# Performance work log

Measured on AMD Instinct MI355X. Metric: run time of the kernel, lower is better.

The kernel has to match this reference:

```python
import jax, jax.numpy as jnp
import numpy as np

NEG_SLOPE = 0.01  # F.leaky_relu default


def grid_sample_bilinear(im, pts):
    """torch.nn.functional.grid_sample equivalent, mode='bilinear',
    align_corners=True, padding_mode='zeros'.
    im: [B, C, H, W], pts: [B, N, 2] in [-1, 1] (x, y order). Returns [B, C, N].
    """
    B, C, H, W = im.shape
    x = (pts[..., 0] + 1.0) * 0.5 * (W - 1)  # [B, N]
    y = (pts[..., 1] + 1.0) * 0.5 * (H - 1)
    x0 = jnp.floor(x)
    y0 = jnp.floor(y)
    wx1 = x - x0
    wy1 = y - y0
    wx0 = 1.0 - wx1
    wy0 = 1.0 - wy1
    x0i = x0.astype(jnp.int32)
    y0i = y0.astype(jnp.int32)
    x1i = x0i + 1
    y1i = y0i + 1

    def corner(yi, xi, w):
        valid = (xi >= 0) & (xi < W) & (yi >= 0) & (yi < H)
        yc = jnp.clip(yi, 0, H - 1)
        xc = jnp.clip(xi, 0, W - 1)
        # gather per-batch: [B, C, N]
        g = jax.vmap(lambda f, yy, xx: f[:, yy, xx])(im, yc, xc)
        return g * (w * valid.astype(im.dtype))[:, None, :]

    return (corner(y0i, x0i, wy0 * wx0) + corner(y0i, x1i, wy0 * wx1)
            + corner(y1i, x0i, wy1 * wx0) + corner(y1i, x1i, wy1 * wx1))


def conv1x1(x, w, b):
    # x: [B, Cin, N], w: [Cout, Cin], b: [Cout] -> [B, Cout, N]
    return jnp.einsum('oi,bin->bon', w, x) + b[None, :, None]


def setup_inputs() -> dict:
    key = jax.random.key(0)
    ks = jax.random.split(key, 9)
    B, N, C, H, W = 64, 6890, 256, 56, 56
    filter_channels = [256, 128, 64, 5]
    points = jax.random.uniform(ks[0], (B, N, 2), jnp.float32, -1.0, 1.0)
    im_feat = jax.random.normal(ks[1], (B, C, H, W), jnp.float32)

    def mk_conv(k, cin, cout):
        k1, k2 = jax.random.split(k)
        bound = 1.0 / np.sqrt(cin)
        w = jax.random.uniform(k1, (cout, cin), jnp.float32, -bound, bound)
        b = jax.random.uniform(k2, (cout,), jnp.float32, -bound, bound)
        return w, b

    w0, b0 = mk_conv(ks[2], filter_channels[0], filter_channels[1])
    w1, b1 = mk_conv(ks[3], filter_channels[1] + filter_channels[0], filter_channels[2])
    w2, b2 = mk_conv(ks[4], filter_channels[2] + filter_channels[0], filter_channels[3])
    return {"points": points, "im_feat": im_feat,
            "w0": w0, "b0": b0, "w1": w1, "b1": b1, "w2": w2, "b2": b2}


def reference(points, im_feat, w0, b0, w1, b1, w2, b2):
    # sampling: bilinear gather of point-wise features, [B, C_s, N]
    point_feat = grid_sample_bilinear(im_feat, points)
    # reduce_dim: 1x1 conv MLP with skip-concat of the input features
    y = jax.nn.leaky_relu(conv1x1(point_feat, w0, b0), NEG_SLOPE)
    y = jax.nn.leaky_relu(conv1x1(jnp.concatenate([y, point_feat], axis=1), w1, b1), NEG_SLOPE)
    y = conv1x1(jnp.concatenate([y, point_feat], axis=1), w2, b2)  # last layer: no leaky_relu
    y = jax.nn.relu(y)  # self.last_op
    mesh_align_feat = y.reshape(y.shape[0], -1)  # [B, C_p * N]
    return (mesh_align_feat, point_feat)
```

## Files before the change

kernel.cpp:

```cpp
#include <hip/hip_runtime.h>

#define B_    64
#define C_    256
#define H_    56
#define W_    56
#define N_    6890
#define HW_   3136
#define NTILE 108
#define GPTS  1723
#define PPT   7

#define WB1_OFF (128*256)
#define WB2_OFF (128*256 + 64*384)
#define WTOT    (128*256 + 64*384 + 5*320)

typedef __attribute__((ext_vector_type(8))) __bf16 bf16x8;
typedef __attribute__((ext_vector_type(8))) unsigned short ushort8;
typedef __attribute__((ext_vector_type(4))) float f32x4;
typedef __attribute__((ext_vector_type(2))) float f32x2;
typedef __attribute__((ext_vector_type(4))) unsigned int uint4v;
typedef __attribute__((ext_vector_type(2))) unsigned int uint2v;

__device__ __forceinline__ unsigned short f2bf(float f) {
    unsigned int u = __builtin_bit_cast(unsigned int, f);
    u += 0x7FFFu + ((u >> 16) & 1u);
    return (unsigned short)(u >> 16);
}
__device__ __forceinline__ unsigned int pack2(float lo, float hi) {
    return (unsigned int)f2bf(lo) | ((unsigned int)f2bf(hi) << 16);
}
__device__ __forceinline__ float leaky(float v) { return v > 0.f ? v : 0.01f * v; }

__global__ void wconv_kernel(const float* __restrict__ w0, const float* __restrict__ w1,
                             const float* __restrict__ w2, unsigned short* __restrict__ wb) {
    int i = blockIdx.x * 256 + threadIdx.x;
    if (i >= WTOT) return;
    float v = (i < WB1_OFF) ? w0[i] : (i < WB2_OFF) ? w1[i - WB1_OFF] : w2[i - WB2_OFF];
    wb[i] = f2bf(v);
}

__device__ __forceinline__ void stage_load(f32x4* rs, const float* src, int t) {
#pragma unroll
    for (int k = 0; k < 13; k++) {
        int idx = t + (k << 8);
        f32x4 z = {0.f, 0.f, 0.f, 0.f};
        rs[k] = (idx < 3136) ? ((const f32x4*)src)[idx] : z;
    }
}
__device__ __forceinline__ void stage_write(float* dst, const f32x4* rs, int t) {
#pragma unroll
    for (int k = 0; k < 13; k++) {
        int idx = t + (k << 8);
        if (idx < 3136) ((f32x4*)dst)[idx] = rs[k];
    }
}

__global__ __launch_bounds__(256) void gather_kernel(
    const float* __restrict__ points, const float* __restrict__ im,
    float* __restrict__ out1) {
    __shared__ float Ls[2][4 * HW_];

    const int t   = threadIdx.x;
    const int bid = blockIdx.x;
    const int xcd  = bid & 7;
    const int slot = bid >> 3;
    const int b    = (slot >> 2) * 8 + xcd;
    const int grp  = slot & 3;
    const int nbase = grp * GPTS;

    int   ia0[PPT], ia1[PPT];
    float wl0[PPT], wr0[PPT], wl1[PPT], wr1[PPT];
#pragma unroll
    for (int p = 0; p < PPT; p++) {
        int ln = t + (p << 8);
        int n  = nbase + ln;
        bool ok = (ln < GPTS) && (n < N_);
        int nl = ok ? n : 0;
        f32x2 pt = *(const f32x2*)(points + ((size_t)b * N_ + nl) * 2);
        float fx = fminf(fmaxf((pt.x + 1.f) * 27.5f, 0.f), 55.f);
        float fy = fminf(fmaxf((pt.y + 1.f) * 27.5f, 0.f), 55.f);
        float x0f = floorf(fx), y0f = floorf(fy);
        int x0 = (int)x0f, y0 = (int)y0f;
        float wx1 = fx - x0f, wy1 = fy - y0f;
        float wx0 = 1.f - wx1, wy0 = 1.f - wy1;
        bool hix = x0 >= W_ - 1;
        int   xb  = hix ? W_ - 2 : x0;
        float wxl = hix ? 0.f : wx0;
        float wxr = hix ? wx0 : wx1;
        int y0c = min(y0, H_ - 1);
        int y1c = min(y0 + 1, H_ - 1);
        float g = ok ? 1.f : 0.f;
        wl0[p] = wy0 * wxl * g; wr0[p] = wy0 * wxr * g;
        wl1[p] = wy1 * wxl * g; wr1[p] = wy1 * wxr * g;
        ia0[p] = y0c * W_ + xb; ia1[p] = y1c * W_ + xb;
    }

    const float* imb = im + (size_t)b * C_ * HW_;
    f32x4 rs[13];

    stage_load(rs, imb, t);
    stage_write(Ls[0], rs, t);
    __syncthreads();

    for (int ch = 0; ch < 64; ch++) {
        const int buf = ch & 1;
        if (ch < 63) stage_load(rs, imb + (size_t)(ch + 1) * 4 * HW_, t);

        const int c0 = ch * 4;
        const float* plane = Ls[buf];
#pragma unroll
        for (int p = 0; p < PPT; p++) {
            int ln = t + (p << 8);
            int n  = nbase + ln;
            bool ok = (ln < GPTS) && (n < N_);
            size_t obase = ((size_t)b * C_ + c0) * N_ + n;
#pragma unroll
            for (int j = 0; j < 4; j++) {
                const float* q = plane + j * HW_;
                float v = wl0[p] * q[ia0[p]] + wr0[p] * q[ia0[p] + 1]
                        + wl1[p] * q[ia1[p]] + wr1[p] * q[ia1[p] + 1];
                if (ok) out1[obase + (size_t)j * N_] = v;
            }
        }
        if (ch < 63) stage_write(Ls[buf ^ 1], rs, t);
        __syncthreads();
    }
}

__device__ __forceinline__ bf16x8 afrag_f32(const float* __restrict__ wp, int ldk,
                                            int rowbase, int k0, int lane, int nrows) {
    int i = rowbase + (lane & 15);
    int k = k0 + ((lane >> 4) << 3);
    ushort8 u;
    if (i < nrows) {
        const float* s = wp + (size_t)i * ldk + k;
#pragma unroll
        for (int j = 0; j < 8; j++) u[j] = f2bf(s[j]);
    } else {
#pragma unroll
        for (int j = 0; j < 8; j++) u[j] = 0;
    }
    return __builtin_bit_cast(bf16x8, u);
}
__device__ __forceinline__ bf16x8 afrag_bf(const unsigned short* __restrict__ wb, int ldk,
                                           int rowbase, int k0, int lane, int nrows) {
    int i = rowbase + (lane & 15);
    int k = k0 + ((lane >> 4) << 3);
    if (i < nrows) return __builtin_bit_cast(bf16x8, *(const ushort8*)(wb + (size_t)i * ldk + k));
    ushort8 z = {0, 0, 0, 0, 0, 0, 0, 0};
    return __builtin_bit_cast(bf16x8, z);
}

__device__ __forceinline__ bf16x8 bfrag(const unsigned int* buf, int rowstride_dw,
                                        int n, int k0) {
    int cd = (k0 >> 1) ^ ((n & 7) << 2);
    uint4v v = *(const uint4v*)(buf + n * rowstride_dw + cd);
    return __builtin_bit_cast(bf16x8, v);
}

template <bool BF16W>
__global__ __launch_bounds__(256) void mlp_kernel(
    const float* __restrict__ pf,
    const float* __restrict__ w0, const float* __restrict__ b0,
    const float* __restrict__ w1, const float* __restrict__ b1,
    const float* __restrict__ w2, const float* __restrict__ b2,
    const unsigned short* __restrict__ wb,
    float* __restrict__ out0) {
    __shared__ unsigned int Xs[64 * 128];
    __shared__ unsigned int Y0s[64 * 64];

    const int t    = threadIdx.x;
    const int lane = t & 63;
    const int wave = t >> 6;
    const int bid  = blockIdx.x;
    const int b    = bid / NTILE;
    const int tile = bid - b * NTILE;
    const int n0   = tile * 64;

    const float* pfb = pf + (size_t)b * C_ * N_;
    const int nn_g = min(n0 + lane, N_ - 1);
    const int swz  = (lane & 7) << 2;
#pragma unroll
    for (int g8 = 0; g8 < 8; g8++) {
        int c0 = wave * 64 + g8 * 8;
        float v[8];
#pragma unroll
        for (int j = 0; j < 8; j++) v[j] = pfb[(size_t)(c0 + j) * N_ + nn_g];
        uint4v pk;
        pk[0] = pack2(v[0], v[1]); pk[1] = pack2(v[2], v[3]);
        pk[2] = pack2(v[4], v[5]); pk[3] = pack2(v[6], v[7]);
        *(uint4v*)(Xs + lane * 128 + ((c0 >> 1) ^ swz)) = pk;
    }

    bf16x8 a1[2][8];
#pragma unroll
    for (int mt = 0; mt < 2; mt++)
#pragma unroll
        for (int ks = 0; ks < 8; ks++)
            a1[mt][ks] = BF16W ? afrag_bf(wb, 256, (wave * 2 + mt) * 16, ks * 32, lane, 1 << 30)
                               : afrag_f32(w0, 256, (wave * 2 + mt) * 16, ks * 32, lane, 1 << 30);

    __syncthreads();

    const int cl = lane & 15;
    const int rh = lane >> 4;
    const int kq = rh << 3;

    f32x4 acc1[2][4] = {};
#pragma unroll
    for (int ks = 0; ks < 8; ks++) {
        bf16x8 bx[4];
#pragma unroll
        for (int nt = 0; nt < 4; nt++)
            bx[nt] = bfrag(Xs, 128, nt * 16 + cl, ks * 32 + kq);
#pragma unroll
        for (int mt = 0; mt < 2; mt++)
#pragma unroll
            for (int nt = 0; nt < 4; nt++)
                acc1[mt][nt] = __builtin_amdgcn_mfma_f32_16x16x32_bf16(
                    a1[mt][ks], bx[nt], acc1[mt][nt], 0, 0, 0);
    }

#pragma unroll
    for (int mt = 0; mt < 2; mt++) {
        int m0 = (wave * 2 + mt) * 16 + (rh << 2);
        f32x4 bias = *(const f32x4*)(b0 + m0);
#pragma unroll
        for (int nt = 0; nt < 4; nt++) {
            int nn = nt * 16 + cl;
            float v0 = leaky(acc1[mt][nt][0] + bias[0]);
            float v1 = leaky(acc1[mt][nt][1] + bias[1]);
            float v2 = leaky(acc1[mt][nt][2] + bias[2]);
            float v3 = leaky(acc1[mt][nt][3] + bias[3]);
            int md = (m0 >> 1) ^ ((nn & 7) << 2);
            uint2v pk; pk[0] = pack2(v0, v1); pk[1] = pack2(v2, v3);
            *(uint2v*)(Y0s + nn * 64 + md) = pk;
        }
    }

    bf16x8 a2[12];
#pragma unroll
    for (int ks = 0; ks < 12; ks++)
        a2[ks] = BF16W ? afrag_bf(wb + WB1_OFF, 384, wave * 16, ks * 32, lane, 1 << 30)
                       : afrag_f32(w1, 384, wave * 16, ks * 32, lane, 1 << 30);

    __syncthreads();

    f32x4 acc2[4] = {};
#pragma unroll
    for (int ks = 0; ks < 12; ks++) {
#pragma unroll
        for (int nt = 0; nt < 4; nt++) {
            bf16x8 bx = (ks < 4) ? bfrag(Y0s, 64, nt * 16 + cl, ks * 32 + kq)
                                 : bfrag(Xs, 128, nt * 16 + cl, (ks - 4) * 32 + kq);
            acc2[nt] = __builtin_amdgcn_mfma_f32_16x16x32_bf16(a2[ks], bx, acc2[nt], 0, 0, 0);
        }
    }

    bf16x8 a3[10];
#pragma unroll
    for (int ks = 0; ks < 10; ks++)
        a3[ks] = BF16W ? afrag_bf(wb + WB2_OFF, 320, 0, ks * 32, lane, 5)
                       : afrag_f32(w2, 320, 0, ks * 32, lane, 5);

    __syncthreads();

    {
        int m0 = wave * 16 + (rh << 2);
        f32x4 bias = *(const f32x4*)(b1 + m0);
#pragma unroll
        for (int nt = 0; nt < 4; nt++) {
            int nn = nt * 16 + cl;
            float v0 = leaky(acc2[nt][0] + bias[0]);
            float v1 = leaky(acc2[nt][1] + bias[1]);
            float v2 = leaky(acc2[nt][2] + bias[2]);
            float v3 = leaky(acc2[nt][3] + bias[3]);
            int md = (m0 >> 1) ^ ((nn & 7) << 2);
            uint2v pk; pk[0] = pack2(v0, v1); pk[1] = pack2(v2, v3);
            *(uint2v*)(Y0s + nn * 32 + md) = pk;
        }
    }

    __syncthreads();

    {
        int nn = wave * 16 + cl;
        f32x4 acc3 = {};
#pragma unroll
        for (int ks = 0; ks < 10; ks++) {
            bf16x8 bx = (ks < 2) ? bfrag(Y0s, 32, nn, ks * 32 + kq)
                                 : bfrag(Xs, 128, nn, (ks - 2) * 32 + kq);
            acc3 = __builtin_amdgcn_mfma_f32_16x16x32_bf16(a3[ks], bx, acc3, 0, 0, 0);
        }
        int gn2 = n0 + nn;
        if (gn2 < N_) {
#pragma unroll
            for (int r = 0; r < 4; r++) {
                int m = (rh << 2) + r;
                if (m < 5) {
                    float v = acc3[r] + b2[m];
                    v = v > 0.f ? v : 0.f;
                    out0[((size_t)b * 5 + m) * N_ + gn2] = v;
                }
            }
        }
    }
}

extern "C" void kernel_launch(void* const* d_in, const int* in_sizes, int n_in,
                              void* d_out, int out_size, void* d_ws, size_t ws_size,
                              hipStream_t stream) {
    const float* points = (const float*)d_in[0];
    const float* im     = (const float*)d_in[1];
    const float* w0     = (const float*)d_in[2];
    const float* b0     = (const float*)d_in[3];
    const float* w1     = (const float*)d_in[4];
    const float* b1     = (const float*)d_in[5];
    const float* w2     = (const float*)d_in[6];
    const float* b2     = (const float*)d_in[7];
    float* out0 = (float*)d_out;
    float* out1 = out0 + (size_t)B_ * 5 * N_;

    const bool use_bf16w = (ws_size >= (size_t)WTOT * 2) && (d_ws != nullptr);
    unsigned short* wb = (unsigned short*)d_ws;

    if (use_bf16w) {
        hipLaunchKernelGGL(wconv_kernel, dim3((WTOT + 255) / 256), dim3(256), 0, stream,
                           w0, w1, w2, wb);
    }
    hipLaunchKernelGGL(gather_kernel, dim3(256), dim3(256), 0, stream,
                       points, im, out1);
    if (use_bf16w) {
        hipLaunchKernelGGL(mlp_kernel<true>, dim3(B_ * NTILE), dim3(256), 0, stream,
                           out1, w0, b0, w1, b1, w2, b2, wb, out0);
    } else {
        hipLaunchKernelGGL(mlp_kernel<false>, dim3(B_ * NTILE), dim3(256), 0, stream,
                           out1, w0, b0, w1, b1, w2, b2, (const unsigned short*)nullptr, out0);
    }
}
```

Measured before the change: 375.8 us.

## Interleave channels in swizzled LDS gather and emit bf16 point features for MLP

New measurement: 482.5 us. 28.4% more time.

```diff
diff --git a/kernel.cpp b/kernel.cpp
--- a/kernel.cpp
+++ b/kernel.cpp
@@ -7,8 +7,9 @@
 #define N_    6890
 #define HW_   3136
 #define NTILE 108
-#define GPTS  1723
-#define PPT   7
+#define GRP_  8
+#define GPTS2 862
+#define PPT2  4
 
 #define WB1_OFF (128*256)
 #define WB2_OFF (128*256 + 64*384)
@@ -30,6 +31,7 @@
     return (unsigned int)f2bf(lo) | ((unsigned int)f2bf(hi) << 16);
 }
 __device__ __forceinline__ float leaky(float v) { return v > 0.f ? v : 0.01f * v; }
+__device__ __forceinline__ int pswz(int p) { return p ^ ((p >> 3) & 7); }
 
 __global__ void wconv_kernel(const float* __restrict__ w0, const float* __restrict__ w1,
                              const float* __restrict__ w2, unsigned short* __restrict__ wb) {
@@ -39,42 +41,27 @@
     wb[i] = f2bf(v);
 }
 
-__device__ __forceinline__ void stage_load(f32x4* rs, const float* src, int t) {
-#pragma unroll
-    for (int k = 0; k < 13; k++) {
-        int idx = t + (k << 8);
-        f32x4 z = {0.f, 0.f, 0.f, 0.f};
-        rs[k] = (idx < 3136) ? ((const f32x4*)src)[idx] : z;
-    }
-}
-__device__ __forceinline__ void stage_write(float* dst, const f32x4* rs, int t) {
-#pragma unroll
-    for (int k = 0; k < 13; k++) {
-        int idx = t + (k << 8);
-        if (idx < 3136) ((f32x4*)dst)[idx] = rs[k];
-    }
-}
-
-__global__ __launch_bounds__(256) void gather_kernel(
+template <bool XP>
+__global__ __launch_bounds__(256, 2) void gather_kernel(
     const float* __restrict__ points, const float* __restrict__ im,
-    float* __restrict__ out1) {
-    __shared__ float Ls[2][4 * HW_];
+    float* __restrict__ out1, unsigned int* __restrict__ x2) {
+    __shared__ float Ls[HW_ * 4];
 
     const int t   = threadIdx.x;
     const int bid = blockIdx.x;
-    const int xcd  = bid & 7;
-    const int slot = bid >> 3;
-    const int b    = (slot >> 2) * 8 + xcd;
-    const int grp  = slot & 3;
-    const int nbase = grp * GPTS;
-
-    int   ia0[PPT], ia1[PPT];
-    float wl0[PPT], wr0[PPT], wl1[PPT], wr1[PPT];
-#pragma unroll
-    for (int p = 0; p < PPT; p++) {
+    const int xcd = bid & 7;
+    const int idx = bid >> 3;
+    const int b   = ((idx & 7) << 3) + xcd;
+    const int grp = idx >> 3;
+    const int nbase = grp * GPTS2;
+
+    int   p00[PPT2], p01[PPT2], p10[PPT2], p11[PPT2];
+    float w00[PPT2], w01[PPT2], w10[PPT2], w11[PPT2];
+#pragma unroll
+    for (int p = 0; p < PPT2; p++) {
         int ln = t + (p << 8);
         int n  = nbase + ln;
-        bool ok = (ln < GPTS) && (n < N_);
+        bool ok = (ln < GPTS2) && (n < N_);
         int nl = ok ? n : 0;
         f32x2 pt = *(const f32x2*)(points + ((size_t)b * N_ + nl) * 2);
         float fx = fminf(fmaxf((pt.x + 1.f) * 27.5f, 0.f), 55.f);
@@ -89,42 +76,75 @@
         float wxr = hix ? wx0 : wx1;
         int y0c = min(y0, H_ - 1);
         int y1c = min(y0 + 1, H_ - 1);
-        float g = ok ? 1.f : 0.f;
-        wl0[p] = wy0 * wxl * g; wr0[p] = wy0 * wxr * g;
-        wl1[p] = wy1 * wxl * g; wr1[p] = wy1 * wxr * g;
-        ia0[p] = y0c * W_ + xb; ia1[p] = y1c * W_ + xb;
-    }
-
-    const float* imb = im + (size_t)b * C_ * HW_;
-    f32x4 rs[13];
-
-    stage_load(rs, imb, t);
-    stage_write(Ls[0], rs, t);
-    __syncthreads();
+        w00[p] = wy0 * wxl; w01[p] = wy0 * wxr;
+        w10[p] = wy1 * wxl; w11[p] = wy1 * wxr;
+        int ia0 = y0c * W_ + xb, ia1 = y1c * W_ + xb;
+        p00[p] = pswz(ia0); p01[p] = pswz(ia0 + 1);
+        p10[p] = pswz(ia1); p11[p] = pswz(ia1 + 1);
+    }
+
+    const f32x4* imb4 = (const f32x4*)(im + (size_t)b * C_ * HW_);
+    f32x4 rs[4][4];
+
+#define GLOAD(CH) {                                                         \
+    _Pragma("unroll")                                                       \
+    for (int k = 0; k < 4; k++) {                                           \
+        int g = t + (k << 8);                                               \
+        if (g < 784) {                                                      \
+            _Pragma("unroll")                                               \
+            for (int j = 0; j < 4; j++)                                     \
+                rs[k][j] = imb4[(size_t)((CH) * 4 + j) * 784 + g];          \
+        }                                                                   \
+    } }
+
+    GLOAD(0);
 
     for (int ch = 0; ch < 64; ch++) {
-        const int buf = ch & 1;
-        if (ch < 63) stage_load(rs, imb + (size_t)(ch + 1) * 4 * HW_, t);
+        __syncthreads();
+#pragma unroll
+        for (int k = 0; k < 4; k++) {
+            int g = t + (k << 8);
+            if (g < 784) {
+#pragma unroll
+                for (int i = 0; i < 4; i++) {
+                    int pi = (g << 2) + i;
+                    f32x4 v = {rs[0][0][0], 0.f, 0.f, 0.f};
+                    v[0] = rs[k][0][i]; v[1] = rs[k][1][i];
+                    v[2] = rs[k][2][i]; v[3] = rs[k][3][i];
+                    *(f32x4*)(Ls + (pswz(pi) << 2)) = v;
+                }
+            }
+        }
+        __syncthreads();
+        if (ch < 63) GLOAD(ch + 1);
 
         const int c0 = ch * 4;
-        const float* plane = Ls[buf];
-#pragma unroll
-        for (int p = 0; p < PPT; p++) {
+#pragma unroll
+        for (int p = 0; p < PPT2; p++) {
+            f32x4 q00 = *(const f32x4*)(Ls + (p00[p] << 2));
+            f32x4 q01 = *(const f32x4*)(Ls + (p01[p] << 2));
+            f32x4 q10 = *(const f32x4*)(Ls + (p10[p] << 2));
+            f32x4 q11 = *(const f32x4*)(Ls + (p11[p] << 2));
+            float v0 = w00[p]*q00[0] + w01[p]*q01[0] + w10[p]*q10[0] + w11[p]*q11[0];
+            float v1 = w00[p]*q00[1] + w01[p]*q01[1] + w10[p]*q10[1] + w11[p]*q11[1];
+            float v2 = w00[p]*q00[2] + w01[p]*q01[2] + w10[p]*q10[2] + w11[p]*q11[2];
+            float v3 = w00[p]*q00[3] + w01[p]*q01[3] + w10[p]*q10[3] + w11[p]*q11[3];
             int ln = t + (p << 8);
             int n  = nbase + ln;
-            bool ok = (ln < GPTS) && (n < N_);
-            size_t obase = ((size_t)b * C_ + c0) * N_ + n;
-#pragma unroll
-            for (int j = 0; j < 4; j++) {
-                const float* q = plane + j * HW_;
-                float v = wl0[p] * q[ia0[p]] + wr0[p] * q[ia0[p] + 1]
-                        + wl1[p] * q[ia1[p]] + wr1[p] * q[ia1[p] + 1];
-                if (ok) out1[obase + (size_t)j * N_] = v;
+            if ((ln < GPTS2) && (n < N_)) {
+                size_t ob = ((size_t)b * C_ + c0) * N_ + n;
+                out1[ob]             = v0;
+                out1[ob + N_]        = v1;
+                out1[ob + 2 * N_]    = v2;
+                out1[ob + 3 * N_]    = v3;
+                if (XP) {
+                    uint2v pk; pk[0] = pack2(v0, v1); pk[1] = pack2(v2, v3);
+                    *(uint2v*)(x2 + ((size_t)((b << 6) + ch) * N_ + n) * 2) = pk;
+                }
             }
         }
-        if (ch < 63) stage_write(Ls[buf ^ 1], rs, t);
-        __syncthreads();
-    }
+    }
+#undef GLOAD
 }
 
 __device__ __forceinline__ bf16x8 afrag_f32(const float* __restrict__ wp, int ldk,
@@ -158,9 +178,9 @@
     return __builtin_bit_cast(bf16x8, v);
 }
 
-template <bool BF16W>
+template <bool XP, bool BF16W>
 __global__ __launch_bounds__(256) void mlp_kernel(
-    const float* __restrict__ pf,
+    const float* __restrict__ pf, const unsigned int* __restrict__ x2,
     const float* __restrict__ w0, const float* __restrict__ b0,
     const float* __restrict__ w1, const float* __restrict__ b1,
     const float* __restrict__ w2, const float* __restrict__ b2,
@@ -177,19 +197,32 @@
     const int tile = bid - b * NTILE;
     const int n0   = tile * 64;
 
-    const float* pfb = pf + (size_t)b * C_ * N_;
     const int nn_g = min(n0 + lane, N_ - 1);
     const int swz  = (lane & 7) << 2;
-#pragma unroll
-    for (int g8 = 0; g8 < 8; g8++) {
-        int c0 = wave * 64 + g8 * 8;
-        float v[8];
-#pragma unroll
-        for (int j = 0; j < 8; j++) v[j] = pfb[(size_t)(c0 + j) * N_ + nn_g];
-        uint4v pk;
-        pk[0] = pack2(v[0], v[1]); pk[1] = pack2(v[2], v[3]);
-        pk[2] = pack2(v[4], v[5]); pk[3] = pack2(v[6], v[7]);
-        *(uint4v*)(Xs + lane * 128 + ((c0 >> 1) ^ swz)) = pk;
+
+    if (XP) {
+#pragma unroll
+        for (int j = 0; j < 8; j++) {
+            int d2a = wave * 16 + 2 * j;
+            const unsigned int* src = x2 + ((size_t)((b << 6) + d2a) * N_ + nn_g) * 2;
+            uint2v q0 = *(const uint2v*)src;
+            uint2v q1 = *(const uint2v*)(src + 2 * (size_t)N_);
+            uint4v pk; pk[0] = q0[0]; pk[1] = q0[1]; pk[2] = q1[0]; pk[3] = q1[1];
+            *(uint4v*)(Xs + lane * 128 + ((wave * 32 + 4 * j) ^ swz)) = pk;
+        }
+    } else {
+        const float* pfb = pf + (size_t)b * C_ * N_;
+#pragma unroll
+        for (int g8 = 0; g8 < 8; g8++) {
+            int c0 = wave * 64 + g8 * 8;
+            float v[8];
+#pragma unroll
+            for (int j = 0; j < 8; j++) v[j] = pfb[(size_t)(c0 + j) * N_ + nn_g];
+            uint4v pk;
+            pk[0] = pack2(v[0], v[1]); pk[1] = pack2(v[2], v[3]);
+            pk[2] = pack2(v[4], v[5]); pk[3] = pack2(v[6], v[7]);
+            *(uint4v*)(Xs + lane * 128 + ((c0 >> 1) ^ swz)) = pk;
+        }
     }
 
     bf16x8 a1[2][8];
@@ -321,20 +354,33 @@
     float* out0 = (float*)d_out;
     float* out1 = out0 + (size_t)B_ * 5 * N_;
 
-    const bool use_bf16w = (ws_size >= (size_t)WTOT * 2) && (d_ws != nullptr);
-    unsigned short* wb = (unsigned short*)d_ws;
-
-    if (use_bf16w) {
+    const size_t XBYTES = (size_t)B_ * 64 * N_ * 2 * 4;
+    const size_t WBYTES = (size_t)WTOT * 2;
+    const bool xok = (d_ws != nullptr) && (ws_size >= XBYTES + WBYTES);
+    const bool wok = xok || ((d_ws != nullptr) && (ws_size >= WBYTES));
+    unsigned int*   x2 = (unsigned int*)d_ws;
+    unsigned short* wb = xok ? (unsigned short*)((char*)d_ws + XBYTES)
+                             : (unsigned short*)d_ws;
+
+    if (wok) {
         hipLaunchKernelGGL(wconv_kernel, dim3((WTOT + 255) / 256), dim3(256), 0, stream,
                            w0, w1, w2, wb);
     }
-    hipLaunchKernelGGL(gather_kernel, dim3(256), dim3(256), 0, stream,
-                       points, im, out1);
-    if (use_bf16w) {
-        hipLaunchKernelGGL(mlp_kernel<true>, dim3(B_ * NTILE), dim3(256), 0, stream,
-                           out1, w0, b0, w1, b1, w2, b2, wb, out0);
+    if (xok) {
+        hipLaunchKernelGGL(gather_kernel<true>, dim3(B_ * GRP_), dim3(256), 0, stream,
+                           points, im, out1, x2);
+        hipLaunchKernelGGL((mlp_kernel<true, true>), dim3(B_ * NTILE), dim3(256), 0, stream,
+                           out1, x2, w0, b0, w1, b1, w2, b2, wb, out0);
     } else {
-        hipLaunchKernelGGL(mlp_kernel<false>, dim3(B_ * NTILE), dim3(256), 0, stream,
-                           out1, w0, b0, w1, b1, w2, b2, (const unsigned short*)nullptr, out0);
-    }
-}
+        hipLaunchKernelGGL(gather_kernel<false>, dim3(B_ * GRP_), dim3(256), 0, stream,
+                           points, im, out1, (unsigned int*)nullptr);
+        if (wok) {
+            hipLaunchKernelGGL((mlp_kernel<false, true>), dim3(B_ * NTILE), dim3(256), 0, stream,
+                               out1, (const unsigned int*)nullptr, w0, b0, w1, b1, w2, b2, wb, out0);
+        } else {
+            hipLaunchKernelGGL((mlp_kernel<false, false>), dim3(B_ * NTILE), dim3(256), 0, stream,
+                               out1, (const unsigned int*)nullptr, w0, b0, w1, b1, w2, b2,
+                               (const unsigned short*)nullptr, out0);
+        }
+    }
+}
```

## Split gather by batch and channel group with interleaved swizzled LDS layout

Applied to the files above, without the earlier changes.

Result: faster. 318.2 us (-15.3%).

```diff
diff --git a/kernel.cpp b/kernel.cpp
--- a/kernel.cpp
+++ b/kernel.cpp
@@ -7,8 +7,6 @@
 #define N_    6890
 #define HW_   3136
 #define NTILE 108
-#define GPTS  1723
-#define PPT   7
 
 #define WB1_OFF (128*256)
 #define WB2_OFF (128*256 + 64*384)
@@ -30,6 +28,7 @@
     return (unsigned int)f2bf(lo) | ((unsigned int)f2bf(hi) << 16);
 }
 __device__ __forceinline__ float leaky(float v) { return v > 0.f ? v : 0.01f * v; }
+__device__ __forceinline__ int pswz(int p) { return p ^ ((p >> 3) & 7); }
 
 __global__ void wconv_kernel(const float* __restrict__ w0, const float* __restrict__ w1,
                              const float* __restrict__ w2, unsigned short* __restrict__ wb) {
@@ -39,91 +38,70 @@
     wb[i] = f2bf(v);
 }
 
-__device__ __forceinline__ void stage_load(f32x4* rs, const float* src, int t) {
-#pragma unroll
-    for (int k = 0; k < 13; k++) {
-        int idx = t + (k << 8);
-        f32x4 z = {0.f, 0.f, 0.f, 0.f};
-        rs[k] = (idx < 3136) ? ((const f32x4*)src)[idx] : z;
-    }
-}
-__device__ __forceinline__ void stage_write(float* dst, const f32x4* rs, int t) {
-#pragma unroll
-    for (int k = 0; k < 13; k++) {
-        int idx = t + (k << 8);
-        if (idx < 3136) ((f32x4*)dst)[idx] = rs[k];
-    }
-}
-
-__global__ __launch_bounds__(256) void gather_kernel(
+__global__ __launch_bounds__(512, 6) void gather_kernel(
     const float* __restrict__ points, const float* __restrict__ im,
     float* __restrict__ out1) {
-    __shared__ float Ls[2][4 * HW_];
+    __shared__ float Ls[HW_ * 4];
 
     const int t   = threadIdx.x;
     const int bid = blockIdx.x;
-    const int xcd  = bid & 7;
-    const int slot = bid >> 3;
-    const int b    = (slot >> 2) * 8 + xcd;
-    const int grp  = slot & 3;
-    const int nbase = grp * GPTS;
-
-    int   ia0[PPT], ia1[PPT];
-    float wl0[PPT], wr0[PPT], wl1[PPT], wr1[PPT];
-#pragma unroll
-    for (int p = 0; p < PPT; p++) {
-        int ln = t + (p << 8);
-        int n  = nbase + ln;
-        bool ok = (ln < GPTS) && (n < N_);
-        int nl = ok ? n : 0;
-        f32x2 pt = *(const f32x2*)(points + ((size_t)b * N_ + nl) * 2);
-        float fx = fminf(fmaxf((pt.x + 1.f) * 27.5f, 0.f), 55.f);
-        float fy = fminf(fmaxf((pt.y + 1.f) * 27.5f, 0.f), 55.f);
-        float x0f = floorf(fx), y0f = floorf(fy);
-        int x0 = (int)x0f, y0 = (int)y0f;
-        float wx1 = fx - x0f, wy1 = fy - y0f;
-        float wx0 = 1.f - wx1, wy0 = 1.f - wy1;
-        bool hix = x0 >= W_ - 1;
-        int   xb  = hix ? W_ - 2 : x0;
-        float wxl = hix ? 0.f : wx0;
-        float wxr = hix ? wx0 : wx1;
-        int y0c = min(y0, H_ - 1);
-        int y1c = min(y0 + 1, H_ - 1);
-        float g = ok ? 1.f : 0.f;
-        wl0[p] = wy0 * wxl * g; wr0[p] = wy0 * wxr * g;
-        wl1[p] = wy1 * wxl * g; wr1[p] = wy1 * wxr * g;
-        ia0[p] = y0c * W_ + xb; ia1[p] = y1c * W_ + xb;
-    }
-
-    const float* imb = im + (size_t)b * C_ * HW_;
-    f32x4 rs[13];
-
-    stage_load(rs, imb, t);
-    stage_write(Ls[0], rs, t);
-    __syncthreads();
-
-    for (int ch = 0; ch < 64; ch++) {
-        const int buf = ch & 1;
-        if (ch < 63) stage_load(rs, imb + (size_t)(ch + 1) * 4 * HW_, t);
-
-        const int c0 = ch * 4;
-        const float* plane = Ls[buf];
-#pragma unroll
-        for (int p = 0; p < PPT; p++) {
-            int ln = t + (p << 8);
-            int n  = nbase + ln;
-            bool ok = (ln < GPTS) && (n < N_);
-            size_t obase = ((size_t)b * C_ + c0) * N_ + n;
-#pragma unroll
-            for (int j = 0; j < 4; j++) {
-                const float* q = plane + j * HW_;
-                float v = wl0[p] * q[ia0[p]] + wr0[p] * q[ia0[p] + 1]
-                        + wl1[p] * q[ia1[p]] + wr1[p] * q[ia1[p] + 1];
-                if (ok) out1[obase + (size_t)j * N_] = v;
+    const int b  = ((bid & 7) << 3) | ((bid >> 3) & 7);
+    const int ch = bid >> 6;
+
+    const f32x4* im4 = (const f32x4*)(im + ((size_t)b * C_ + ch * 4) * HW_);
+#pragma unroll
+    for (int g0 = 0; g0 < 2; g0++) {
+        int g = t + (g0 << 9);
+        if (g < 784) {
+            f32x4 r0 = im4[g];
+            f32x4 r1 = im4[784 + g];
+            f32x4 r2 = im4[1568 + g];
+            f32x4 r3 = im4[2352 + g];
+#pragma unroll
+            for (int i = 0; i < 4; i++) {
+                f32x4 v; v[0] = r0[i]; v[1] = r1[i]; v[2] = r2[i]; v[3] = r3[i];
+                *(f32x4*)(Ls + (pswz((g << 2) + i) << 2)) = v;
             }
         }
-        if (ch < 63) stage_write(Ls[buf ^ 1], rs, t);
-        __syncthreads();
+    }
+    __syncthreads();
+
+    const float* ptb = points + (size_t)b * N_ * 2;
+    const size_t ob0 = ((size_t)b * C_ + ch * 4) * N_;
+#pragma unroll 2
+    for (int p = 0; p < 14; p++) {
+        int n = t + (p << 9);
+        if (n < N_) {
+            f32x2 pt = *(const f32x2*)(ptb + 2 * n);
+            float fx = fminf(fmaxf((pt.x + 1.f) * 27.5f, 0.f), 55.f);
+            float fy = fminf(fmaxf((pt.y + 1.f) * 27.5f, 0.f), 55.f);
+            float x0f = floorf(fx), y0f = floorf(fy);
+            int x0 = (int)x0f, y0 = (int)y0f;
+            float wx1 = fx - x0f, wy1 = fy - y0f;
+            float wx0 = 1.f - wx1, wy0 = 1.f - wy1;
+            bool hix = x0 >= W_ - 1;
+            int   xb  = hix ? W_ - 2 : x0;
+            float wxl = hix ? 0.f : wx0;
+            float wxr = hix ? wx0 : wx1;
+            int y0c = min(y0, H_ - 1);
+            int y1c = min(y0 + 1, H_ - 1);
+            float w00 = wy0 * wxl, w01 = wy0 * wxr;
+            float w10 = wy1 * wxl, w11 = wy1 * wxr;
+            int ia0 = y0c * W_ + xb, ia1 = y1c * W_ + xb;
+
+            f32x4 q00 = *(const f32x4*)(Ls + (pswz(ia0)     << 2));
+            f32x4 q01 = *(const f32x4*)(Ls + (pswz(ia0 + 1) << 2));
+            f32x4 q10 = *(const f32x4*)(Ls + (pswz(ia1)     << 2));
+            f32x4 q11 = *(const f32x4*)(Ls + (pswz(ia1 + 1) << 2));
+            float v0 = w00*q00[0] + w01*q01[0] + w10*q10[0] + w11*q11[0];
+            float v1 = w00*q00[1] + w01*q01[1] + w10*q10[1] + w11*q11[1];
+            float v2 = w00*q00[2] + w01*q01[2] + w10*q10[2] + w11*q11[2];
+            float v3 = w00*q00[3] + w01*q01[3] + w10*q10[3] + w11*q11[3];
+            out1[ob0 + n]          = v0;
+            out1[ob0 + N_ + n]     = v1;
+            out1[ob0 + 2*N_ + n]   = v2;
+            out1[ob0 + 3*N_ + n]   = v3;
+        }
     }
 }
 
@@ -177,9 +155,10 @@
     const int tile = bid - b * NTILE;
     const int n0   = tile * 64;
 
-    const float* pfb = pf + (size_t)b * C_ * N_;
     const int nn_g = min(n0 + lane, N_ - 1);
     const int swz  = (lane & 7) << 2;
+
+    const float* pfb = pf + (size_t)b * C_ * N_;
 #pragma unroll
     for (int g8 = 0; g8 < 8; g8++) {
         int c0 = wave * 64 + g8 * 8;
@@ -321,16 +300,17 @@
     float* out0 = (float*)d_out;
     float* out1 = out0 + (size_t)B_ * 5 * N_;
 
-    const bool use_bf16w = (ws_size >= (size_t)WTOT * 2) && (d_ws != nullptr);
+    const size_t WBYTES = (size_t)WTOT * 2;
+    const bool wok = (d_ws != nullptr) && (ws_size >= WBYTES);
     unsigned short* wb = (unsigned short*)d_ws;
 
-    if (use_bf16w) {
+    if (wok) {
         hipLaunchKernelGGL(wconv_kernel, dim3((WTOT + 255) / 256), dim3(256), 0, stream,
                            w0, w1, w2, wb);
     }
-    hipLaunchKernelGGL(gather_kernel, dim3(256), dim3(256), 0, stream,
+    hipLaunchKernelGGL(gather_kernel, dim3(B_ * 64), dim3(512), 0, stream,
                        points, im, out1);
-    if (use_bf16w) {
+    if (wok) {
         hipLaunchKernelGGL(mlp_kernel<true>, dim3(B_ * NTILE), dim3(256), 0, stream,
                            out1, w0, b0, w1, b1, w2, b2, wb, out0);
     } else {
```
